# Performance work log

Measured on AMD Instinct MI355X. Metric: run time of the kernel, lower is better.

The kernel has to match this reference:

```python
import jax, jax.numpy as jnp
import numpy as np

B, DX, DY = 128, 3, 3
D = DX * DY          # max_digit = 9
N = D * D            # num_nodes = 81
HID = 96
EMB = 16
ITERS = 4
M = B * N * D        # LSTM flattened rows = 93312


def _sudoku_adj():
    idx = np.arange(N)
    r, c = idx // D, idx % D
    br, bc = r // DX, c // DY
    same = (r[:, None] == r[None]) | (c[:, None] == c[None]) | ((br[:, None] == br[None]) & (bc[:, None] == bc[None]))
    return (same & ~np.eye(N, dtype=bool)).astype(np.float32)


def setup_inputs() -> dict:
    key = jax.random.key(0)
    ks = iter(jax.random.split(key, 40))

    def dense(shape, fan_in):
        return jax.random.normal(next(ks), shape, jnp.float32) / np.float32(np.sqrt(fan_in))

    return {
        "inputs": jax.random.randint(next(ks), (B, N), 0, D + 1, jnp.int32),
        "c0": jax.random.normal(next(ks), (M, HID), jnp.float32),
        "adj_cell": jnp.asarray((np.ones((D, D)) - np.eye(D)).astype(np.float32)),
        "adj_digit": jnp.asarray(_sudoku_adj()),
        "enc_W1": dense((3, EMB), 3), "enc_b1": jnp.zeros((EMB,), jnp.float32),
        "enc_W2": dense((EMB, HID), EMB), "enc_b2": jnp.zeros((HID,), jnp.float32),
        "cr_W": dense((3, HID, HID), HID), "cr_b": jnp.zeros((3, HID), jnp.float32),
        "dr_W": dense((3, HID, HID), HID), "dr_b": jnp.zeros((3, HID), jnp.float32),
        "gm_W1": dense((3 * HID, HID), 3 * HID), "gm_b1": jnp.zeros((HID,), jnp.float32),
        "gm_W2": dense((2, HID, HID), HID), "gm_b2": jnp.zeros((2, HID), jnp.float32),
        "lstm_Wih": dense((4 * HID, HID), HID), "lstm_Whh": dense((4 * HID, HID), HID),
        "lstm_bih": jnp.zeros((4 * HID,), jnp.float32), "lstm_bhh": jnp.zeros((4 * HID,), jnp.float32),
        "r_W12": dense((2, HID, HID), HID), "r_b12": jnp.zeros((2, HID), jnp.float32),
        "r_W3": dense((HID, 1), HID), "r_b3": jnp.zeros((1,), jnp.float32),
        "iters": ITERS,
    }


def _mlp(x, Ws, bs):
    # stacked MLP: ReLU between layers, none after the last
    L = Ws.shape[0]
    for l in range(L):
        x = x @ Ws[l] + bs[l]
        if l < L - 1:
            x = jax.nn.relu(x)
    return x


def _forward(inputs, c0, adj_cell, adj_digit, enc_W1, enc_b1, enc_W2, enc_b2,
             cr_W, cr_b, dr_W, dr_b, gm_W1, gm_b1, gm_W2, gm_b2,
             lstm_Wih, lstm_Whh, lstm_bih, lstm_bhh, r_W12, r_b12, r_W3, r_b3, iters):
    # mask: [B,N,D,3] = (blank, equals digit d+1, filled-with-other-digit)
    eq = inputs[:, :, None] == jnp.arange(1, D + 1, dtype=inputs.dtype)[None, None, :]
    given = inputs != 0
    mask = jnp.stack([
        jnp.broadcast_to((~given)[:, :, None], eq.shape), eq,
        (~eq) & given[:, :, None]
    ], axis=-1).astype(jnp.float32)

    X = jax.nn.relu(mask @ enc_W1 + enc_b1) @ enc_W2 + enc_b2  # [B,N,D,HID]

    def lstm_step(x, h, c):
        gates = x @ lstm_Wih.T + lstm_bih + h @ lstm_Whh.T + lstm_bhh
        i, f, g, o = jnp.split(gates, 4, axis=-1)  # PyTorch gate order i,f,g,o
        c = jax.nn.sigmoid(f) * c + jax.nn.sigmoid(i) * jnp.tanh(g)
        h = jax.nn.sigmoid(o) * jnp.tanh(c)
        return h, c

    def step(carry, _):
        h, c = carry  # [M,HID] each
        Hn = h.reshape(X.shape)
        # relational message passing: per-node MLP then sum over graph edges
        msg_cell = jnp.einsum('bndh,de->bneh', _mlp(Hn, cr_W, cr_b), adj_cell)
        msg_digit = jnp.einsum('bndh,nm->bmdh', _mlp(Hn, dr_W, dr_b), adj_digit)
        g = jnp.concatenate([X, msg_cell, msg_digit], axis=-1)  # [B,N,D,3*HID]
        g = jax.nn.relu(g @ gm_W1 + gm_b1)
        g = jax.nn.relu(g @ gm_W2[0] + gm_b2[0])
        g = g @ gm_W2[1] + gm_b2[1]
        h, c = lstm_step(g.reshape(-1, HID), h, c)
        Hn = h.reshape(X.shape)
        out = jax.nn.relu(Hn @ r_W12[0] + r_b12[0])
        out = jax.nn.relu(out @ r_W12[1] + r_b12[1])
        out = (out @ r_W3 + r_b3)[..., 0]  # [B,N,D]
        return (h, c), out

    (_, _), outs = jax.lax.scan(step, (X.reshape(-1, HID), c0), None, length=iters)
    return outs  # [iters,B,N,D]


def reference(inputs, c0, adj_cell, adj_digit, enc_W1, enc_b1, enc_W2, enc_b2,
              cr_W, cr_b, dr_W, dr_b, gm_W1, gm_b1, gm_W2, gm_b2,
              lstm_Wih, lstm_Whh, lstm_bih, lstm_bhh, r_W12, r_b12, r_W3, r_b3, iters):
    return _forward(inputs, c0, adj_cell, adj_digit, enc_W1, enc_b1, enc_W2, enc_b2,
                    cr_W, cr_b, dr_W, dr_b, gm_W1, gm_b1, gm_W2, gm_b2,
                    lstm_Wih, lstm_Whh, lstm_bih, lstm_bhh, r_W12, r_b12, r_W3, r_b3, iters)
```

## Files before the change

kernel.cpp:

```cpp
#include <hip/hip_runtime.h>
#include <hip/hip_bf16.h>

typedef unsigned short u16;
typedef __bf16 bf16x8 __attribute__((ext_vector_type(8)));
typedef float  f32x4  __attribute__((ext_vector_type(4)));
typedef u16    u16x8  __attribute__((ext_vector_type(8)));

#define HID   96
#define LDP   104
#define MROWS 93312
#define BN    10368
#define GRID_TILE 1458
#define LSTM_GRID 5832
#define SGS   104

#define FCH 9216

#define MFMA(a,b,c) __builtin_amdgcn_mfma_f32_16x16x32_bf16((a),(b),(c),0,0,0)

__device__ __forceinline__ float bf2f(u16 x){
  union { float f; unsigned u; } v; v.u = ((unsigned)x) << 16; return v.f;
}
__device__ __forceinline__ u16 f2bf(float f){
  union { float f; unsigned u; } v; v.f = f;
  unsigned r = v.u + 0x7fffu + ((v.u >> 16) & 1u);
  return (u16)(r >> 16);
}
__device__ __forceinline__ float sigf(float x){ return 1.f/(1.f + __expf(-x)); }
__device__ __forceinline__ float tanhf_(float x){
  float xx = fminf(fmaxf(x, -15.f), 15.f);
  float e = __expf(-2.f * xx);
  return (1.f - e) / (1.f + e);
}
__device__ __forceinline__ void lds_fence(){
  asm volatile("s_waitcnt lgkmcnt(0)" ::: "memory");
}

struct Frags { bf16x8 a0, a1, a2; };

__device__ __forceinline__ Frags load_afrags_g(const u16* __restrict__ A, size_t row0, int lane){
  int t16 = lane & 15, q = lane >> 4;
  const u16* p = A + (row0 + (size_t)t16) * 96 + q * 8;
  Frags f;
  f.a0 = *reinterpret_cast<const bf16x8*>(p);
  f.a1 = *reinterpret_cast<const bf16x8*>(p + 32);
  f.a2 = *reinterpret_cast<const bf16x8*>(p + 64);
  return f;
}
__device__ __forceinline__ Frags load_afrags_s(const u16* sA, int row0, int lane){
  int t16 = lane & 15, q = lane >> 4;
  const u16* p = sA + (row0 + t16) * LDP + q * 8;
  Frags f;
  f.a0 = *reinterpret_cast<const bf16x8*>(p);
  f.a1 = *reinterpret_cast<const bf16x8*>(p + 32);
  f.a2 = *reinterpret_cast<const bf16x8*>(p + 64);
  return f;
}

__device__ __forceinline__ void layer_g(Frags f, const u16* __restrict__ wb,
    const float* __restrict__ bias, u16* dst, int dstStride, size_t rowBase,
    bool relu, int lane)
{
  int t16 = lane & 15, q = lane >> 4;
  #pragma unroll
  for (int nt = 0; nt < 6; nt++){
    float b = bias ? bias[nt * 16 + t16] : 0.f;
    f32x4 acc = {b, b, b, b};
    const u16* wp = wb + nt * 1536 + lane * 8;
    acc = MFMA(f.a0, *reinterpret_cast<const bf16x8*>(wp),        acc);
    acc = MFMA(f.a1, *reinterpret_cast<const bf16x8*>(wp + 512),  acc);
    acc = MFMA(f.a2, *reinterpret_cast<const bf16x8*>(wp + 1024), acc);
    #pragma unroll
    for (int j = 0; j < 4; j++){
      float v = acc[j];
      if (relu) v = fmaxf(v, 0.f);
      dst[(rowBase + q * 4 + j) * (size_t)dstStride + nt * 16 + t16] = f2bf(v);
    }
  }
}

__device__ __forceinline__ void mfma6_g(f32x4* acc, int tbase, Frags f,
    const u16* __restrict__ wb, int lane)
{
  #pragma unroll
  for (int jt = 0; jt < 6; jt++){
    const u16* wp = wb + jt * 1536 + lane * 8;
    acc[tbase + jt] = MFMA(f.a0, *reinterpret_cast<const bf16x8*>(wp),        acc[tbase + jt]);
    acc[tbase + jt] = MFMA(f.a1, *reinterpret_cast<const bf16x8*>(wp + 512),  acc[tbase + jt]);
    acc[tbase + jt] = MFMA(f.a2, *reinterpret_cast<const bf16x8*>(wp + 1024), acc[tbase + jt]);
  }
}

__global__ __launch_bounds__(256) void k_prep2(const float* __restrict__ crW,
    const float* __restrict__ drW, const float* __restrict__ gmW1,
    const float* __restrict__ gmW2, const float* __restrict__ rW12,
    const float* __restrict__ Wih, const float* __restrict__ Whh,
    u16* __restrict__ pWB)
{
  int b = blockIdx.x, tid = threadIdx.x;
  u16* dst = pWB + b * FCH;
  if (b < 12){
    const float* src;
    if (b < 3)       src = crW  + b * 9216;
    else if (b < 6)  src = drW  + (b - 3) * 9216;
    else if (b == 6) src = gmW1 + 9216;
    else if (b == 7) src = gmW1 + 18432;
    else if (b < 10) src = gmW2 + (b - 8) * 9216;
    else             src = rW12 + (b - 10) * 9216;
    #pragma unroll
    for (int i = 0; i < 36; i++){
      int idx = tid + i * 256;
      int f = idx >> 9, rem = idx & 511, l = rem >> 3, j = rem & 7;
      int nt = f / 3, kc = f - nt * 3;
      int n = nt * 16 + (l & 15);
      int k = ((l >> 4) << 3) + kc * 32 + j;
      dst[idx] = f2bf(src[k * 96 + n]);
    }
  } else {
    int bb = b - 12;
    const float* src = (bb < 4 ? Wih : Whh) + (bb & 3) * 9216;
    #pragma unroll
    for (int i = 0; i < 36; i++){
      int idx = tid + i * 256;
      int f = idx >> 9, rem = idx & 511, l = rem >> 3, j = rem & 7;
      int nt = f / 3, kc = f - nt * 3;
      int n = nt * 16 + (l & 15);
      int k = ((l >> 4) << 3) + kc * 32 + j;
      dst[idx] = f2bf(src[n * 96 + k]);
    }
  }
}

__global__ void k_tables(const float* __restrict__ eW1, const float* __restrict__ eb1,
                         const float* __restrict__ eW2, const float* __restrict__ eb2,
                         const float* __restrict__ gmW1, const float* __restrict__ gmb1,
                         const float* __restrict__ bih, const float* __restrict__ bhh,
                         float* __restrict__ XTab, float* __restrict__ XgTab,
                         float* __restrict__ bsum)
{
  __shared__ float sX[3][96];
  int j = threadIdx.x;
  for (int n = j; n < 384; n += 128) bsum[n] = bih[n] + bhh[n];
  if (j < 96){
    for (int ch = 0; ch < 3; ch++){
      float acc = eb2[j];
      for (int e = 0; e < 16; e++){
        float hv = fmaxf(eW1[ch * 16 + e] + eb1[e], 0.f);
        acc += hv * eW2[e * 96 + j];
      }
      sX[ch][j] = acc;
      XTab[ch * 96 + j] = acc;
    }
  }
  __syncthreads();
  if (j < 96){
    for (int ch = 0; ch < 3; ch++){
      float acc = gmb1[j];
      for (int k = 0; k < 96; k++) acc += sX[ch][k] * gmW1[k * 96 + j];
      XgTab[ch * 96 + j] = acc;
    }
  }
}

__global__ __launch_bounds__(256) void k_init(const int* __restrict__ inputs,
    const float* __restrict__ XTab, u16* __restrict__ h)
{
  int idx = blockIdx.x * 256 + threadIdx.x;
  int m = idx / 12, h8 = idx - m * 12;
  int bn = m / 9, d = m - bn * 9;
  int inp = inputs[bn];
  int ch = (inp == 0) ? 0 : ((inp == d + 1) ? 1 : 2);
  const float* xt = XTab + ch * 96 + h8 * 8;
  u16* hp = h + (size_t)m * 96 + h8 * 8;
  #pragma unroll
  for (int e = 0; e < 8; e++) hp[e] = f2bf(xt[e]);
}

__global__ __launch_bounds__(256) void k_ab3(const u16* __restrict__ h,
    u16* __restrict__ Y, u16* __restrict__ Z,
    const u16* __restrict__ pWB, const float* __restrict__ crB,
    const float* __restrict__ drB)
{
  __shared__ u16 sA[64 * LDP];
  const int tid = threadIdx.x, lane = tid & 63, wave = tid >> 6;
  const int wrow = wave * 16;
  const size_t rbase = (size_t)blockIdx.x * 64;

  Frags hf = load_afrags_g(h, rbase + wrow, lane);

  layer_g(hf, pWB, crB, sA, LDP, wrow, true, lane);                  lds_fence();
  Frags f = load_afrags_s(sA, wrow, lane);
  layer_g(f, pWB + 1 * FCH, crB + 96, sA, LDP, wrow, true, lane);    lds_fence();
  f = load_afrags_s(sA, wrow, lane);
  layer_g(f, pWB + 2 * FCH, crB + 192, sA, LDP, wrow, false, lane);  lds_fence();
  f = load_afrags_s(sA, wrow, lane);
  layer_g(f, pWB + 6 * FCH, nullptr, Y, 96, rbase + wrow, false, lane);
  lds_fence();

  layer_g(hf, pWB + 3 * FCH, drB, sA, LDP, wrow, true, lane);        lds_fence();
  f = load_afrags_s(sA, wrow, lane);
  layer_g(f, pWB + 4 * FCH, drB + 96, sA, LDP, wrow, true, lane);    lds_fence();
  f = load_afrags_s(sA, wrow, lane);
  layer_g(f, pWB + 5 * FCH, drB + 192, sA, LDP, wrow, false, lane);  lds_fence();
  f = load_afrags_s(sA, wrow, lane);
  layer_g(f, pWB + 7 * FCH, nullptr, Z, 96, rbase + wrow, false, lane);
}

__device__ __forceinline__ void addrow(float* s, const u16* p){
  u16x8 t = *reinterpret_cast<const u16x8*>(p);
  #pragma unroll
  for (int e = 0; e < 8; e++) s[e] += bf2f(t[e]);
}

__global__ __launch_bounds__(256) void k_msg(u16* __restrict__ Z,
    const u16* __restrict__ Y, u16* __restrict__ Ssum)
{
  __shared__ u16 sT[81 * LDP];
  const int tid = threadIdx.x;
  if (blockIdx.x >= 1152){
    int idx = (blockIdx.x - 1152) * 256 + tid;
    int bn = idx / 12, h8 = idx - bn * 12;
    const u16* base = Y + (size_t)bn * 864 + h8 * 8;
    float s[8];
    #pragma unroll
    for (int e = 0; e < 8; e++) s[e] = 0.f;
    #pragma unroll
    for (int d = 0; d < 9; d++){
      u16x8 v = *reinterpret_cast<const u16x8*>(base + d * 96);
      #pragma unroll
      for (int e = 0; e < 8; e++) s[e] += bf2f(v[e]);
    }
    u16x8 o;
    #pragma unroll
    for (int e = 0; e < 8; e++) o[e] = f2bf(s[e]);
    *reinterpret_cast<u16x8*>(Ssum + (size_t)bn * 96 + h8 * 8) = o;
    return;
  }
  const int b = blockIdx.x / 9, d = blockIdx.x - b * 9;
  const size_t base = ((size_t)b * 729 + d) * 96;
  for (int i = tid; i < 972; i += 256){
    int n = i / 12, k8 = i - n * 12;
    *reinterpret_cast<u16x8*>(sT + n * LDP + k8 * 8) =
      *reinterpret_cast<const u16x8*>(Z + base + (size_t)n * 864 + k8 * 8);
  }
  __syncthreads();
  for (int i = tid; i < 972; i += 256){
    int m = i / 12, k8 = i - m * 12;
    int r = m / 9, cc = m - r * 9;
    int br = (r / 3) * 3, bc = (cc / 3) * 3;
    float s[8];
    #pragma unroll
    for (int e = 0; e < 8; e++) s[e] = 0.f;
    #pragma unroll
    for (int c2 = 0; c2 < 9; c2++) if (c2 != cc) addrow(s, sT + (r * 9 + c2) * LDP + k8 * 8);
    #pragma unroll
    for (int r2 = 0; r2 < 9; r2++) if (r2 != r) addrow(s, sT + (r2 * 9 + cc) * LDP + k8 * 8);
    #pragma unroll
    for (int r2 = 0; r2 < 3; r2++)
      #pragma unroll
      for (int c2 = 0; c2 < 3; c2++){
        int rr = br + r2, c3 = bc + c2;
        if (rr != r && c3 != cc) addrow(s, sT + (rr * 9 + c3) * LDP + k8 * 8);
      }
    u16x8 o;
    #pragma unroll
    for (int e = 0; e < 8; e++) o[e] = f2bf(s[e]);
    *reinterpret_cast<u16x8*>(Z + base + (size_t)m * 864 + k8 * 8) = o;
  }
}

__global__ __launch_bounds__(256) void k_glr_a(u16* YG,
    const u16* __restrict__ Zd, const u16* __restrict__ Ssum,
    const int* __restrict__ inputs, const float* __restrict__ XgTab,
    const u16* __restrict__ pWB, const float* __restrict__ gmb2)
{
  __shared__ u16 sA[64 * LDP];
  const int tid = threadIdx.x, lane = tid & 63, wave = tid >> 6;
  const int wrow = wave * 16;
  const size_t rbase = (size_t)blockIdx.x * 64;

  for (int i = lane; i < 192; i += 64){
    int rl = i / 12, kc = i - rl * 12;
    int m = (int)rbase + wrow + rl;
    int bn = m / 9, d = m - bn * 9;
    int inp = inputs[bn];
    int ch = (inp == 0) ? 0 : ((inp == d + 1) ? 1 : 2);
    const float* xg = XgTab + ch * 96 + kc * 8;
    u16x8 vy = *reinterpret_cast<const u16x8*>(YG   + (size_t)m * 96 + kc * 8);
    u16x8 vz = *reinterpret_cast<const u16x8*>(Zd   + (size_t)m * 96 + kc * 8);
    u16x8 vs = *reinterpret_cast<const u16x8*>(Ssum + (size_t)bn * 96 + kc * 8);
    u16x8 o;
    #pragma unroll
    for (int e = 0; e < 8; e++)
      o[e] = f2bf(fmaxf(xg[e] + bf2f(vs[e]) - bf2f(vy[e]) + bf2f(vz[e]), 0.f));
    *reinterpret_cast<u16x8*>(sA + (wrow + rl) * LDP + kc * 8) = o;
  }
  lds_fence();

  Frags f = load_afrags_s(sA, wrow, lane);
  layer_g(f, pWB + 8 * FCH, gmb2, sA, LDP, wrow, true, lane);        lds_fence();
  f = load_afrags_s(sA, wrow, lane);
  layer_g(f, pWB + 9 * FCH, gmb2 + 96, YG, 96, rbase + wrow, false, lane);
}

__global__ __launch_bounds__(256, 8) void k_lstm(const u16* __restrict__ G,
    u16* h, const float* __restrict__ cin, float* __restrict__ cout,
    const float* __restrict__ bsum, const u16* __restrict__ pWB)
{
  __shared__ float sG[4][16][SGS];
  const int tid = threadIdx.x, lane = tid & 63, w = tid >> 6;
  const int t16 = lane & 15, q = lane >> 4;
  const size_t rbase = (size_t)blockIdx.x * 16;

  f32x4 acc[6];
  #pragma unroll
  for (int nt = 0; nt < 6; nt++){
    float b = bsum[w * 96 + nt * 16 + t16];
    f32x4 a = {b, b, b, b};
    acc[nt] = a;
  }
  Frags aG = load_afrags_g(G, rbase, lane);
  mfma6_g(acc, 0, aG, pWB + (12 + w) * FCH, lane);
  Frags ah = load_afrags_g(h, rbase, lane);
  mfma6_g(acc, 0, ah, pWB + (16 + w) * FCH, lane);

  #pragma unroll
  for (int nt = 0; nt < 6; nt++)
    #pragma unroll
    for (int j = 0; j < 4; j++)
      sG[w][q * 4 + j][nt * 16 + t16] = acc[nt][j];
  __syncthreads();

  #pragma unroll
  for (int e = 0; e < 6; e++){
    int idx = e * 256 + tid;
    int r = idx / 96, col = idx - r * 96;
    float iv = sG[0][r][col];
    float fv = sG[1][r][col];
    float gv = sG[2][r][col];
    float ov = sG[3][r][col];
    size_t m = rbase + r;
    float cn = sigf(fv) * cin[m * 96 + col] + sigf(iv) * tanhf_(gv);
    float hn = sigf(ov) * tanhf_(cn);
    cout[m * 96 + col] = cn;
    h[m * 96 + col] = f2bf(hn);
  }
}

__global__ __launch_bounds__(256) void k_read(const u16* __restrict__ h,
    const u16* __restrict__ pWB, const float* __restrict__ rb12,
    const float* __restrict__ rW3, const float* __restrict__ rb3,
    float* __restrict__ out)
{
  __shared__ u16 sA[64 * LDP];
  const int tid = threadIdx.x, lane = tid & 63, wave = tid >> 6;
  const int wrow = wave * 16;
  const size_t rbase = (size_t)blockIdx.x * 64;

  Frags f = load_afrags_g(h, rbase + wrow, lane);
  layer_g(f, pWB + 10 * FCH, rb12, sA, LDP, wrow, true, lane);       lds_fence();
  f = load_afrags_s(sA, wrow, lane);
  layer_g(f, pWB + 11 * FCH, rb12 + 96, sA, LDP, wrow, true, lane);  lds_fence();

  int row = tid >> 2, part = tid & 3;
  float s = 0.f;
  const u16* rp = sA + row * LDP + part * 24;
  #pragma unroll
  for (int k = 0; k < 24; k++) s += bf2f(rp[k]) * rW3[part * 24 + k];
  s += __shfl_xor(s, 1);
  s += __shfl_xor(s, 2);
  if (part == 0) out[rbase + row] = s + rb3[0];
}

extern "C" void kernel_launch(void* const* d_in, const int* in_sizes, int n_in,
                              void* d_out, int out_size, void* d_ws, size_t ws_size,
                              hipStream_t stream)
{
  (void)in_sizes; (void)n_in; (void)out_size; (void)ws_size;
  const int*   inputs = (const int*)d_in[0];
  const float* c0     = (const float*)d_in[1];
  const float* eW1  = (const float*)d_in[4];
  const float* eb1  = (const float*)d_in[5];
  const float* eW2  = (const float*)d_in[6];
  const float* eb2  = (const float*)d_in[7];
  const float* crW  = (const float*)d_in[8];
  const float* crB  = (const float*)d_in[9];
  const float* drW  = (const float*)d_in[10];
  const float* drB  = (const float*)d_in[11];
  const float* gmW1 = (const float*)d_in[12];
  const float* gmb1 = (const float*)d_in[13];
  const float* gmW2 = (const float*)d_in[14];
  const float* gmb2 = (const float*)d_in[15];
  const float* Wih  = (const float*)d_in[16];
  const float* Whh  = (const float*)d_in[17];
  const float* bih  = (const float*)d_in[18];
  const float* bhh  = (const float*)d_in[19];
  const float* rW12 = (const float*)d_in[20];
  const float* rb12 = (const float*)d_in[21];
  const float* rW3  = (const float*)d_in[22];
  const float* rb3  = (const float*)d_in[23];

  char* ws = (char*)d_ws;
  float* XgTab = (float*)(ws);
  float* XTab  = (float*)(ws + 4096);
  float* bsum  = (float*)(ws + 6144);
  u16*   pWB   = (u16*)(ws + 8192);
  u16* h  = (u16*)(ws + 8192 + 401408);
  u16* B1 = h  + (size_t)MROWS * 96;
  u16* B2 = B1 + (size_t)MROWS * 96;
  float* c = (float*)(B2 + (size_t)MROWS * 96);
  u16* Ssum = (u16*)(c + (size_t)MROWS * 96);
  float* out = (float*)d_out;

  k_prep2<<<20, 256, 0, stream>>>(crW, drW, gmW1, gmW2, rW12, Wih, Whh, pWB);
  k_tables<<<1, 128, 0, stream>>>(eW1, eb1, eW2, eb2, gmW1, gmb1, bih, bhh,
                                  XTab, XgTab, bsum);
  k_init<<<(MROWS * 12) / 256, 256, 0, stream>>>(inputs, XTab, h);

  for (int it = 0; it < 4; ++it){
    const float* cin = (it == 0) ? c0 : c;
    k_ab3<<<GRID_TILE, 256, 0, stream>>>(h, B1, B2, pWB, crB, drB);
    k_msg<<<1152 + 486, 256, 0, stream>>>(B2, B1, Ssum);
    k_glr_a<<<GRID_TILE, 256, 0, stream>>>(B1, B2, Ssum, inputs, XgTab, pWB, gmb2);
    k_lstm<<<LSTM_GRID, 256, 0, stream>>>(B1, h, cin, c, bsum, pWB);
    k_read<<<GRID_TILE, 256, 0, stream>>>(h, pWB, rb12, rW3, rb3,
                                          out + (size_t)it * MROWS);
  }
}
```

Baseline: 701.6 us.

## Fold last gated-MLP linear layer into LSTM input weights

The final linear layer of the gate MLP (gmW2[1], no activation) is algebraically merged into the LSTM input projection. A new prep kernel computes the product of gmW2[1] and Wih^T, and the bias folds gmb2[1]·Wih into the LSTM bias. k_glr_a drops one 96x96 matmul per iteration and k_lstm reads the ReLU output directly. The change also swaps divisions for hardware reciprocal in sigmoid/tanh and prefetches the cell state early in k_lstm. Folding the weights changes rounding because the combined weight is quantized to bf16 once instead of passing through an intermediate bf16 activation.

```diff
diff --git a/kernel.cpp b/kernel.cpp
--- a/kernel.cpp
+++ b/kernel.cpp
@@ -26,11 +26,12 @@
   unsigned r = v.u + 0x7fffu + ((v.u >> 16) & 1u);
   return (u16)(r >> 16);
 }
-__device__ __forceinline__ float sigf(float x){ return 1.f/(1.f + __expf(-x)); }
+__device__ __forceinline__ float frcp(float x){ return __builtin_amdgcn_rcpf(x); }
+__device__ __forceinline__ float sigf(float x){ return frcp(1.f + __expf(-x)); }
 __device__ __forceinline__ float tanhf_(float x){
   float xx = fminf(fmaxf(x, -15.f), 15.f);
   float e = __expf(-2.f * xx);
-  return (1.f - e) / (1.f + e);
+  return (1.f - e) * frcp(1.f + e);
 }
 __device__ __forceinline__ void lds_fence(){
   asm volatile("s_waitcnt lgkmcnt(0)" ::: "memory");
@@ -94,12 +95,11 @@
 __global__ __launch_bounds__(256) void k_prep2(const float* __restrict__ crW,
     const float* __restrict__ drW, const float* __restrict__ gmW1,
     const float* __restrict__ gmW2, const float* __restrict__ rW12,
-    const float* __restrict__ Wih, const float* __restrict__ Whh,
-    u16* __restrict__ pWB)
+    const float* __restrict__ Whh, u16* __restrict__ pWB)
 {
   int b = blockIdx.x, tid = threadIdx.x;
-  u16* dst = pWB + b * FCH;
   if (b < 12){
+    u16* dst = pWB + b * FCH;
     const float* src;
     if (b < 3)       src = crW  + b * 9216;
     else if (b < 6)  src = drW  + (b - 3) * 9216;
@@ -118,7 +118,8 @@
     }
   } else {
     int bb = b - 12;
-    const float* src = (bb < 4 ? Wih : Whh) + (bb & 3) * 9216;
+    u16* dst = pWB + (16 + bb) * FCH;
+    const float* src = Whh + bb * 9216;
     #pragma unroll
     for (int i = 0; i < 36; i++){
       int idx = tid + i * 256;
@@ -131,16 +132,44 @@
   }
 }
 
+__global__ __launch_bounds__(256) void k_prepf(const float* __restrict__ gmW2,
+    const float* __restrict__ Wih, u16* __restrict__ pWB)
+{
+  __shared__ float sW[9216];
+  int g = blockIdx.x, tid = threadIdx.x;
+  for (int i = tid; i < 9216; i += 256) sW[i] = gmW2[9216 + i];
+  __syncthreads();
+  u16* dst = pWB + (12 + g) * FCH;
+  #pragma unroll 2
+  for (int i = 0; i < 36; i++){
+    int idx = tid + i * 256;
+    int f = idx >> 9, rem = idx & 511, l = rem >> 3, j = rem & 7;
+    int nt = f / 3, kc = f - nt * 3;
+    int n = nt * 16 + (l & 15);
+    int k = ((l >> 4) << 3) + kc * 32 + j;
+    const float* wr = Wih + (g * 96 + n) * 96;
+    float acc = 0.f;
+    for (int jj = 0; jj < 96; jj++) acc += sW[k * 96 + jj] * wr[jj];
+    dst[idx] = f2bf(acc);
+  }
+}
+
 __global__ void k_tables(const float* __restrict__ eW1, const float* __restrict__ eb1,
                          const float* __restrict__ eW2, const float* __restrict__ eb2,
                          const float* __restrict__ gmW1, const float* __restrict__ gmb1,
                          const float* __restrict__ bih, const float* __restrict__ bhh,
+                         const float* __restrict__ gmb2, const float* __restrict__ Wih,
                          float* __restrict__ XTab, float* __restrict__ XgTab,
-                         float* __restrict__ bsum)
+                         float* __restrict__ bsx)
 {
   __shared__ float sX[3][96];
   int j = threadIdx.x;
-  for (int n = j; n < 384; n += 128) bsum[n] = bih[n] + bhh[n];
+  for (int n = j; n < 384; n += 128){
+    float acc = bih[n] + bhh[n];
+    const float* wr = Wih + n * 96;
+    for (int jj = 0; jj < 96; jj++) acc += gmb2[96 + jj] * wr[jj];
+    bsx[n] = acc;
+  }
   if (j < 96){
     for (int ch = 0; ch < 3; ch++){
       float acc = eb2[j];
@@ -298,28 +327,34 @@
   lds_fence();
 
   Frags f = load_afrags_s(sA, wrow, lane);
-  layer_g(f, pWB + 8 * FCH, gmb2, sA, LDP, wrow, true, lane);        lds_fence();
-  f = load_afrags_s(sA, wrow, lane);
-  layer_g(f, pWB + 9 * FCH, gmb2 + 96, YG, 96, rbase + wrow, false, lane);
-}
-
-__global__ __launch_bounds__(256, 8) void k_lstm(const u16* __restrict__ G,
-    u16* h, const float* __restrict__ cin, float* __restrict__ cout,
-    const float* __restrict__ bsum, const u16* __restrict__ pWB)
+  layer_g(f, pWB + 8 * FCH, gmb2, YG, 96, rbase + wrow, true, lane);
+}
+
+__global__ __launch_bounds__(256, 8) void k_lstm(const u16* __restrict__ A1,
+    u16* h, const float* cin, float* cout,
+    const float* __restrict__ bsx, const u16* __restrict__ pWB)
 {
   __shared__ float sG[4][16][SGS];
   const int tid = threadIdx.x, lane = tid & 63, w = tid >> 6;
   const int t16 = lane & 15, q = lane >> 4;
   const size_t rbase = (size_t)blockIdx.x * 16;
 
+  float cpre[6];
+  #pragma unroll
+  for (int e = 0; e < 6; e++){
+    int idx = e * 256 + tid;
+    int r = idx / 96, col = idx - r * 96;
+    cpre[e] = cin[(rbase + r) * 96 + col];
+  }
+
   f32x4 acc[6];
   #pragma unroll
   for (int nt = 0; nt < 6; nt++){
-    float b = bsum[w * 96 + nt * 16 + t16];
+    float b = bsx[w * 96 + nt * 16 + t16];
     f32x4 a = {b, b, b, b};
     acc[nt] = a;
   }
-  Frags aG = load_afrags_g(G, rbase, lane);
+  Frags aG = load_afrags_g(A1, rbase, lane);
   mfma6_g(acc, 0, aG, pWB + (12 + w) * FCH, lane);
   Frags ah = load_afrags_g(h, rbase, lane);
   mfma6_g(acc, 0, ah, pWB + (16 + w) * FCH, lane);
@@ -340,7 +375,7 @@
     float gv = sG[2][r][col];
     float ov = sG[3][r][col];
     size_t m = rbase + r;
-    float cn = sigf(fv) * cin[m * 96 + col] + sigf(iv) * tanhf_(gv);
+    float cn = sigf(fv) * cpre[e] + sigf(iv) * tanhf_(gv);
     float hn = sigf(ov) * tanhf_(cn);
     cout[m * 96 + col] = cn;
     h[m * 96 + col] = f2bf(hn);
@@ -403,7 +438,7 @@
   char* ws = (char*)d_ws;
   float* XgTab = (float*)(ws);
   float* XTab  = (float*)(ws + 4096);
-  float* bsum  = (float*)(ws + 6144);
+  float* bsx   = (float*)(ws + 6144);
   u16*   pWB   = (u16*)(ws + 8192);
   u16* h  = (u16*)(ws + 8192 + 401408);
   u16* B1 = h  + (size_t)MROWS * 96;
@@ -412,9 +447,10 @@
   u16* Ssum = (u16*)(c + (size_t)MROWS * 96);
   float* out = (float*)d_out;
 
-  k_prep2<<<20, 256, 0, stream>>>(crW, drW, gmW1, gmW2, rW12, Wih, Whh, pWB);
+  k_prep2<<<16, 256, 0, stream>>>(crW, drW, gmW1, gmW2, rW12, Whh, pWB);
+  k_prepf<<<4, 256, 0, stream>>>(gmW2, Wih, pWB);
   k_tables<<<1, 128, 0, stream>>>(eW1, eb1, eW2, eb2, gmW1, gmb1, bih, bhh,
-                                  XTab, XgTab, bsum);
+                                  gmb2, Wih, XTab, XgTab, bsx);
   k_init<<<(MROWS * 12) / 256, 256, 0, stream>>>(inputs, XTab, h);
 
   for (int it = 0; it < 4; ++it){
@@ -422,7 +458,7 @@
     k_ab3<<<GRID_TILE, 256, 0, stream>>>(h, B1, B2, pWB, crB, drB);
     k_msg<<<1152 + 486, 256, 0, stream>>>(B2, B1, Ssum);
     k_glr_a<<<GRID_TILE, 256, 0, stream>>>(B1, B2, Ssum, inputs, XgTab, pWB, gmb2);
-    k_lstm<<<LSTM_GRID, 256, 0, stream>>>(B1, h, cin, c, bsum, pWB);
+    k_lstm<<<LSTM_GRID, 256, 0, stream>>>(B1, h, cin, c, bsx, pWB);
     k_read<<<GRID_TILE, 256, 0, stream>>>(h, pWB, rb12, rW3, rb3,
                                           out + (size_t)it * MROWS);
   }
```

Result: slower. 716.0 us (+2.1%).
